# Optimization experiments

Hardware: AMD Instinct MI355X
Metric: run time of the kernel (lower is better)

Reference implementation:

```python
import jax, jax.numpy as jnp
import numpy as np

BETA = 0.25
ALPHA = 0.5
K = 1024
D = 64


def setup_inputs() -> dict:
    key = jax.random.key(0)
    k1, k2 = jax.random.split(key)
    latents = jax.random.normal(k1, (32, D, 64, 64), dtype=jnp.float32)  # NCHW
    # nn.Embedding init uniform_(-1/K, 1/K)
    emb_weight = jax.random.uniform(k2, (K, D), dtype=jnp.float32, minval=-1.0 / K, maxval=1.0 / K)
    return {"latents": latents, "emb_weight": emb_weight}


def reference(latents, emb_weight):
    # NCHW -> NHWC
    x = jnp.transpose(latents, (0, 2, 3, 1))  # [B,H,W,D]
    B, H, W, Dd = x.shape
    flat = x.reshape(-1, Dd)  # [N,D]

    dist = (jnp.sum(flat * flat, axis=1, keepdims=True)
            + jnp.sum(emb_weight * emb_weight, axis=1)
            - 2.0 * flat @ emb_weight.T)
    inds = jnp.argmin(dist, axis=1)  # [N]

    # one-hot @ W == gather
    q = emb_weight[inds].reshape(B, H, W, Dd)

    commitment_loss = jnp.mean((jax.lax.stop_gradient(q) - x) ** 2)
    embedding_loss = jnp.mean((q - jax.lax.stop_gradient(x)) ** 2)
    vq_loss = commitment_loss * BETA + embedding_loss * ALPHA

    alpha_q = 2.0 * ALPHA / (B * H * W * Dd)
    q_st = x + alpha_q * q + jax.lax.stop_gradient((1.0 - alpha_q) * q - x)

    out = jnp.transpose(q_st, (0, 3, 1, 2))  # NHWC -> NCHW
    return out, vq_loss, inds.reshape(B, H, W)
```

## Files before the change

kernel.cpp:

```cpp
#include <hip/hip_runtime.h>

typedef __attribute__((ext_vector_type(8))) short bf16x8;
typedef __attribute__((ext_vector_type(4))) float f32x4;
typedef __attribute__((ext_vector_type(4))) int   i32x4;

#define NROWS     131072
#define KCODES    1024
#define OUT_ELEMS 8388608
#define RPB       64
#define NBLK      2048
#define MAGICF    12582912.0f
#define MARGIN    240
#define XSTRIDE   67
#define WS_PART   0
#define WS_SE     (16*1024)
#define WS_SEM    (20*1024)
#define WS_BPREP  (24*1024)

__device__ __forceinline__ float pairwise64_sq(const float* __restrict__ v) {
#pragma clang fp contract(off)
    float r[8];
#pragma unroll
    for (int j = 0; j < 8; ++j) r[j] = v[j] * v[j];
#pragma unroll
    for (int i = 8; i < 64; i += 8) {
#pragma unroll
        for (int j = 0; j < 8; ++j) r[j] += v[i + j] * v[i + j];
    }
    return ((r[0] + r[1]) + (r[2] + r[3])) + ((r[4] + r[5]) + (r[6] + r[7]));
}

__device__ __forceinline__ int med3i(int a, int b, int c) {
    int mn = min(a, b), mx = max(a, b);
    return max(mn, min(mx, c));
}

__device__ __forceinline__ unsigned short rne_bf16(float v) {
    unsigned u = __float_as_uint(v);
    return (unsigned short)((u + 0x7fffu + ((u >> 16) & 1u)) >> 16);
}

__global__ __launch_bounds__(256) void vq_prep(
    const float* __restrict__ emb, float* __restrict__ se,
    float* __restrict__ sem, unsigned short* __restrict__ bprep)
{
#pragma clang fp contract(off)
    const int k = blockIdx.x * 256 + threadIdx.x;
    if (k >= KCODES) return;
    const float* e = emb + (k << 6);
    float s = pairwise64_sq(e);
    se[k]  = s;
    sem[k] = (s * 65536.0f) + MAGICF;

    const int c = k >> 4, slot = k & 15;
#pragma unroll
    for (int f = 0; f < 2; ++f) {
#pragma unroll
        for (int g = 0; g < 4; ++g) {
            unsigned short h[8];
#pragma unroll
            for (int j = 0; j < 8; ++j)
                h[j] = rne_bf16(e[f * 32 + g * 8 + j] * 256.0f);
            int4 w;
            w.x = h[0] | (h[1] << 16); w.y = h[2] | (h[3] << 16);
            w.z = h[4] | (h[5] << 16); w.w = h[6] | (h[7] << 16);
            *reinterpret_cast<int4*>(bprep + (((c * 2 + f) * 64 + (g * 16 + slot)) << 3)) = w;
        }
    }
}

__global__ __launch_bounds__(256, 2) void vq_main(
    const float* __restrict__ lat, const float* __restrict__ emb,
    const float* __restrict__ se_g, const float* __restrict__ sem_g,
    const unsigned short* __restrict__ bprep,
    float* __restrict__ out, double* __restrict__ partials)
{
#pragma clang fp contract(off)
    __shared__ float  x_lds[RPB * XSTRIDE];
    __shared__ float  se_lds[KCODES];
    __shared__ float  sem_lds[KCODES];
    __shared__ int    keys_lds[RPB * 49];
    __shared__ int    idx_lds[RPB];
    __shared__ double wsum[4];

    const int tid = threadIdx.x, l = tid & 63, wv = tid >> 6;
    const int blk = blockIdx.x;
    const int n0 = blk * RPB, b = n0 >> 12, hw0 = n0 & 4095;
    const float* latb = lat + ((size_t)b << 18) + hw0;

    {
        const int row = tid & 63, dbase = (tid >> 6) * 16;
#pragma unroll
        for (int dd = 0; dd < 16; ++dd) {
            int d = dbase + dd;
            x_lds[row * XSTRIDE + d] = latb[((size_t)d << 12) + row];
        }
    }
    for (int i = tid; i < KCODES; i += 256) { se_lds[i] = se_g[i]; sem_lds[i] = sem_g[i]; }
    __syncthreads();

    bf16x8 afrag[2];
    {
        const int arow = l & 15, kb = (l >> 4) << 3;
        const float* xr = x_lds + (wv * 16 + arow) * XSTRIDE;
#pragma unroll
        for (int kh = 0; kh < 2; ++kh) {
            bf16x8 f;
#pragma unroll
            for (int j = 0; j < 8; ++j)
                f[j] = (short)rne_bf16(xr[kh * 32 + kb + j] * -512.0f);
            afrag[kh] = f;
        }
    }

    int m1[4], m2[4], m3[4];
#pragma unroll
    for (int r = 0; r < 4; ++r) { m1[r] = m2[r] = m3[r] = 0x7fffffff; }

    const i32x4* bp = reinterpret_cast<const i32x4*>(bprep);
    i32x4 bbuf[2][2];
    bbuf[0][0] = bp[l];
    bbuf[0][1] = bp[64 + l];

#pragma unroll 2
    for (int c = 0; c < 64; ++c) {
        const int cur = c & 1, nxt = cur ^ 1;
        if (c < 63) {
            bbuf[nxt][0] = bp[(c + 1) * 128 + l];
            bbuf[nxt][1] = bp[(c + 1) * 128 + 64 + l];
        }
        const float sevm = sem_lds[c * 16 + (l & 15)];
        bf16x8 b0 = __builtin_bit_cast(bf16x8, bbuf[cur][0]);
        bf16x8 b1 = __builtin_bit_cast(bf16x8, bbuf[cur][1]);
        const unsigned code0 = (unsigned)((c << 4) + (l & 15));
        f32x4 acc = {0.f, 0.f, 0.f, 0.f};
        acc = __builtin_amdgcn_mfma_f32_16x16x32_bf16(afrag[0], b0, acc, 0, 0, 0);
        acc = __builtin_amdgcn_mfma_f32_16x16x32_bf16(afrag[1], b1, acc, 0, 0, 0);
#pragma unroll
        for (int r = 0; r < 4; ++r) {
            float uf = acc[r] + sevm;
            int key = (int)((__float_as_uint(uf) << 10) | code0);
            int n1 = min(key, m1[r]);
            int n2 = med3i(key, m1[r], m2[r]);
            int n3 = med3i(max(key, m1[r]), m2[r], m3[r]);
            m1[r] = n1; m2[r] = n2; m3[r] = n3;
        }
    }

#pragma unroll
    for (int r = 0; r < 4; ++r) {
        const int rloc = wv * 16 + ((l >> 4) << 2) + r;
        keys_lds[rloc * 49 + (l & 15) * 3 + 0] = m1[r];
        keys_lds[rloc * 49 + (l & 15) * 3 + 1] = m2[r];
        keys_lds[rloc * 49 + (l & 15) * 3 + 2] = m3[r];
    }
    __syncthreads();

    {
        const int row = tid >> 2, h = tid & 3;
        const int kbase = row * 49 + h * 12;
        int mk = 0x7fffffff;
#pragma unroll
        for (int i = 0; i < 12; ++i) mk = min(mk, keys_lds[kbase + i]);
        mk = min(mk, __shfl_xor(mk, 1, 64));
        mk = min(mk, __shfl_xor(mk, 2, 64));
        const int lim = mk + (MARGIN << 10) + 1023;

        const float* xr = x_lds + row * XSTRIDE;
        float rr0 = 0.0f, rr1 = 0.0f;
#pragma unroll
        for (int i = 0; i < 64; i += 8) {
            float v0 = xr[i + 2 * h];
            float v1 = xr[i + 2 * h + 1];
            rr0 += v0 * v0;
            rr1 += v1 * v1;
        }
        float s_h = rr0 + rr1;
        float p   = s_h + __shfl_xor(s_h, 1, 64);
        float sx  = p + __shfl_xor(p, 2, 64);

        float bestd = 3.4e38f; int besti = KCODES;
#pragma unroll 4
        for (int i = 0; i < 12; ++i) {
            int key = keys_lds[kbase + i];
            if (key <= lim) {
                int code = key & 1023;
                const float* e = emb + (code << 6);
                float g = 0.0f;
#pragma unroll
                for (int d = 0; d < 64; ++d)
                    g = fmaf(xr[d], e[d], g);
                float ss   = sx + se_lds[code];
                float dist = ss - 2.0f * g;
                if (dist < bestd || (dist == bestd && code < besti)) { bestd = dist; besti = code; }
            }
        }
#pragma unroll
        for (int off = 1; off <= 2; off <<= 1) {
            float od = __shfl_xor(bestd, off, 64);
            int   oi = __shfl_xor(besti, off, 64);
            if (od < bestd || (od == bestd && oi < besti)) { bestd = od; besti = oi; }
        }
        if (h == 0) {
            idx_lds[row] = besti;
            out[OUT_ELEMS + 1 + (size_t)n0 + row] = (float)besti;
        }
    }
    __syncthreads();

    double lsum = 0.0;
    {
        const float aq = 1.0f / 8388608.0f;
        const int row = tid & 63, dh = (tid >> 6) * 16;
        const int code = idx_lds[row];
        const float4* eq4 = reinterpret_cast<const float4*>(emb + (code << 6) + dh);
        const float* xr = x_lds + row * XSTRIDE;
        float* ob = out + ((size_t)b << 18) + hw0 + row;
#pragma unroll
        for (int qq = 0; qq < 4; ++qq) {
            float4 qv = eq4[qq];
            float qa[4] = {qv.x, qv.y, qv.z, qv.w};
#pragma unroll
            for (int u = 0; u < 4; ++u) {
                int d = dh + qq * 4 + u;
                float xv = xr[d];
                float qd = qa[u];
                float v  = (xv + aq * qd) + ((1.0f - aq) * qd - xv);
                ob[(size_t)d << 12] = v;
                float diff = qd - xv;
                lsum += (double)diff * (double)diff;
            }
        }
    }

#pragma unroll
    for (int off = 32; off > 0; off >>= 1) lsum += __shfl_down(lsum, off, 64);
    if (l == 0) wsum[wv] = lsum;
    __syncthreads();
    if (tid == 0) partials[blk] = (wsum[0] + wsum[1]) + (wsum[2] + wsum[3]);
}

__global__ __launch_bounds__(512) void vq_finish(
    const double* __restrict__ partials, float* __restrict__ out)
{
    __shared__ double lds[8];
    const int t = threadIdx.x;
    double s = ((partials[t] + partials[t + 512]) + partials[t + 1024]) + partials[t + 1536];
#pragma unroll
    for (int off = 32; off > 0; off >>= 1) s += __shfl_down(s, off, 64);
    if ((t & 63) == 0) lds[t >> 6] = s;
    __syncthreads();
    if (t == 0) {
        double tot = 0.0;
#pragma unroll
        for (int i = 0; i < 8; ++i) tot += lds[i];
        out[OUT_ELEMS] = (float)(0.75 * tot / (double)OUT_ELEMS);
    }
}

extern "C" void kernel_launch(void* const* d_in, const int* in_sizes, int n_in,
                              void* d_out, int out_size, void* d_ws, size_t ws_size,
                              hipStream_t stream)
{
    const float* lat = (const float*)d_in[0];
    const float* emb = (const float*)d_in[1];
    float* out = (float*)d_out;
    char* ws = (char*)d_ws;

    double* partials      = (double*)(ws + WS_PART);
    float* se             = (float*)(ws + WS_SE);
    float* sem            = (float*)(ws + WS_SEM);
    unsigned short* bprep = (unsigned short*)(ws + WS_BPREP);

    vq_prep<<<dim3(4),    dim3(256), 0, stream>>>(emb, se, sem, bprep);
    vq_main<<<dim3(NBLK), dim3(256), 0, stream>>>(lat, emb, se, sem, bprep, out, partials);
    vq_finish<<<dim3(1),  dim3(512), 0, stream>>>(partials, out);
}
```

Baseline: 97.02 us.

## Stage codebook tiles into LDS with async global_load_lds double buffering

```diff
diff --git a/kernel.cpp b/kernel.cpp
--- a/kernel.cpp
+++ b/kernel.cpp
@@ -14,7 +14,7 @@
 #define XSTRIDE   67
 #define WS_PART   0
 #define WS_SE     (16*1024)
-#define WS_SEM    (20*1024)
+#define WS_SEMG   (20*1024)
 #define WS_BPREP  (24*1024)
 
 __device__ __forceinline__ float pairwise64_sq(const float* __restrict__ v) {
@@ -42,15 +42,15 @@
 
 __global__ __launch_bounds__(256) void vq_prep(
     const float* __restrict__ emb, float* __restrict__ se,
-    float* __restrict__ sem, unsigned short* __restrict__ bprep)
+    float* __restrict__ semg, unsigned short* __restrict__ bprep)
 {
 #pragma clang fp contract(off)
     const int k = blockIdx.x * 256 + threadIdx.x;
     if (k >= KCODES) return;
     const float* e = emb + (k << 6);
     float s = pairwise64_sq(e);
-    se[k]  = s;
-    sem[k] = (s * 65536.0f) + MAGICF;
+    se[k]   = s;
+    semg[k] = MAGICF + s * 65536.0f;
 
     const int c = k >> 4, slot = k & 15;
 #pragma unroll
@@ -71,15 +71,14 @@
 
 __global__ __launch_bounds__(256, 2) void vq_main(
     const float* __restrict__ lat, const float* __restrict__ emb,
-    const float* __restrict__ se_g, const float* __restrict__ sem_g,
+    const float* __restrict__ se_g, const float* __restrict__ semg_g,
     const unsigned short* __restrict__ bprep,
     float* __restrict__ out, double* __restrict__ partials)
 {
 #pragma clang fp contract(off)
     __shared__ float  x_lds[RPB * XSTRIDE];
-    __shared__ float  se_lds[KCODES];
-    __shared__ float  sem_lds[KCODES];
     __shared__ int    keys_lds[RPB * 49];
+    __shared__ i32x4  stage4[512];
     __shared__ int    idx_lds[RPB];
     __shared__ double wsum[4];
 
@@ -87,6 +86,15 @@
     const int blk = blockIdx.x;
     const int n0 = blk * RPB, b = n0 >> 12, hw0 = n0 & 4095;
     const float* latb = lat + ((size_t)b << 18) + hw0;
+    const char* bpb = (const char*)bprep;
+    const int scol = l & 15;
+
+#define STAGE(P, S)                                                              \
+    __builtin_amdgcn_global_load_lds(                                            \
+        (const __attribute__((address_space(1))) unsigned int*)                  \
+            (bpb + ((P) * 4096 + wv * 1024 + l * 16)),                           \
+        (__attribute__((address_space(3))) unsigned int*)                        \
+            (&stage4[(S) * 256 + wv * 64]), 16, 0, 0)
 
     {
         const int row = tid & 63, dbase = (tid >> 6) * 16;
@@ -96,56 +104,70 @@
             x_lds[row * XSTRIDE + d] = latb[((size_t)d << 12) + row];
         }
     }
-    for (int i = tid; i < KCODES; i += 256) { se_lds[i] = se_g[i]; sem_lds[i] = sem_g[i]; }
-    __syncthreads();
-
-    bf16x8 afrag[2];
+    STAGE(0, 0);
+    __syncthreads();
+
+    bf16x8 afrag0, afrag1;
     {
         const int arow = l & 15, kb = (l >> 4) << 3;
         const float* xr = x_lds + (wv * 16 + arow) * XSTRIDE;
-#pragma unroll
-        for (int kh = 0; kh < 2; ++kh) {
-            bf16x8 f;
-#pragma unroll
-            for (int j = 0; j < 8; ++j)
-                f[j] = (short)rne_bf16(xr[kh * 32 + kb + j] * -512.0f);
-            afrag[kh] = f;
-        }
+        bf16x8 f;
+#pragma unroll
+        for (int j = 0; j < 8; ++j) f[j] = (short)rne_bf16(xr[kb + j]      * -512.0f);
+        afrag0 = f;
+#pragma unroll
+        for (int j = 0; j < 8; ++j) f[j] = (short)rne_bf16(xr[32 + kb + j] * -512.0f);
+        afrag1 = f;
     }
 
     int m1[4], m2[4], m3[4];
 #pragma unroll
     for (int r = 0; r < 4; ++r) { m1[r] = m2[r] = m3[r] = 0x7fffffff; }
 
-    const i32x4* bp = reinterpret_cast<const i32x4*>(bprep);
-    i32x4 bbuf[2][2];
-    bbuf[0][0] = bp[l];
-    bbuf[0][1] = bp[64 + l];
-
-#pragma unroll 2
-    for (int c = 0; c < 64; ++c) {
-        const int cur = c & 1, nxt = cur ^ 1;
-        if (c < 63) {
-            bbuf[nxt][0] = bp[(c + 1) * 128 + l];
-            bbuf[nxt][1] = bp[(c + 1) * 128 + 64 + l];
-        }
-        const float sevm = sem_lds[c * 16 + (l & 15)];
-        bf16x8 b0 = __builtin_bit_cast(bf16x8, bbuf[cur][0]);
-        bf16x8 b1 = __builtin_bit_cast(bf16x8, bbuf[cur][1]);
-        const unsigned code0 = (unsigned)((c << 4) + (l & 15));
-        f32x4 acc = {0.f, 0.f, 0.f, 0.f};
-        acc = __builtin_amdgcn_mfma_f32_16x16x32_bf16(afrag[0], b0, acc, 0, 0, 0);
-        acc = __builtin_amdgcn_mfma_f32_16x16x32_bf16(afrag[1], b1, acc, 0, 0, 0);
-#pragma unroll
-        for (int r = 0; r < 4; ++r) {
-            float uf = acc[r] + sevm;
-            int key = (int)((__float_as_uint(uf) << 10) | code0);
-            int n1 = min(key, m1[r]);
-            int n2 = med3i(key, m1[r], m2[r]);
-            int n3 = med3i(max(key, m1[r]), m2[r], m3[r]);
-            m1[r] = n1; m2[r] = n2; m3[r] = n3;
-        }
-    }
+    float svA0 = semg_g[scol],            svB0 = semg_g[16 + scol];
+    float svA1 = semg_g[32 + scol],       svB1 = semg_g[48 + scol];
+
+#define CHUNK(S, CI, CC, SV)                                                          \
+    {   i32x4 B0 = stage4[(S) * 256 + (CI) * 128 + l];                                \
+        i32x4 B1 = stage4[(S) * 256 + (CI) * 128 + 64 + l];                           \
+        bf16x8 b0_ = __builtin_bit_cast(bf16x8, B0);                                  \
+        bf16x8 b1_ = __builtin_bit_cast(bf16x8, B1);                                  \
+        const unsigned code0_ = (unsigned)(((CC) << 4) + scol);                       \
+        f32x4 acc = {SV, SV, SV, SV};                                                 \
+        acc = __builtin_amdgcn_mfma_f32_16x16x32_bf16(afrag0, b0_, acc, 0, 0, 0);     \
+        acc = __builtin_amdgcn_mfma_f32_16x16x32_bf16(afrag1, b1_, acc, 0, 0, 0);     \
+        _Pragma("unroll")                                                             \
+        for (int r = 0; r < 4; ++r) {                                                 \
+            int key = (int)((__float_as_uint(acc[r]) << 10) | code0_);                \
+            int n1 = min(key, m1[r]);                                                 \
+            int n2 = med3i(key, m1[r], m2[r]);                                        \
+            int n3 = med3i(max(key, m1[r]), m2[r], m3[r]);                            \
+            m1[r] = n1; m2[r] = n2; m3[r] = n3;                                       \
+        }                                                                             \
+    }
+
+#pragma unroll 1
+    for (int p = 0; p < 32; p += 2) {
+        if (p + 1 < 32) STAGE(p + 1, 1);
+        CHUNK(0, 0, 2 * p,     svA0);
+        CHUNK(0, 1, 2 * p + 1, svB0);
+        if (p + 2 < 32) {
+            svA0 = semg_g[(2 * p + 4) * 16 + scol];
+            svB0 = semg_g[(2 * p + 5) * 16 + scol];
+        }
+        __syncthreads();
+
+        if (p + 2 < 32) STAGE(p + 2, 0);
+        CHUNK(1, 0, 2 * p + 2, svA1);
+        CHUNK(1, 1, 2 * p + 3, svB1);
+        if (p + 3 < 32) {
+            svA1 = semg_g[(2 * p + 6) * 16 + scol];
+            svB1 = semg_g[(2 * p + 7) * 16 + scol];
+        }
+        __syncthreads();
+    }
+#undef CHUNK
+#undef STAGE
 
 #pragma unroll
     for (int r = 0; r < 4; ++r) {
@@ -176,8 +198,8 @@
             rr1 += v1 * v1;
         }
         float s_h = rr0 + rr1;
-        float p   = s_h + __shfl_xor(s_h, 1, 64);
-        float sx  = p + __shfl_xor(p, 2, 64);
+        float pq  = s_h + __shfl_xor(s_h, 1, 64);
+        float sx  = pq + __shfl_xor(pq, 2, 64);
 
         float bestd = 3.4e38f; int besti = KCODES;
 #pragma unroll 4
@@ -190,7 +212,7 @@
 #pragma unroll
                 for (int d = 0; d < 64; ++d)
                     g = fmaf(xr[d], e[d], g);
-                float ss   = sx + se_lds[code];
+                float ss   = sx + se_g[code];
                 float dist = ss - 2.0f * g;
                 if (dist < bestd || (dist == bestd && code < besti)) { bestd = dist; besti = code; }
             }
@@ -269,10 +291,10 @@
 
     double* partials      = (double*)(ws + WS_PART);
     float* se             = (float*)(ws + WS_SE);
-    float* sem            = (float*)(ws + WS_SEM);
+    float* semg           = (float*)(ws + WS_SEMG);
     unsigned short* bprep = (unsigned short*)(ws + WS_BPREP);
 
-    vq_prep<<<dim3(4),    dim3(256), 0, stream>>>(emb, se, sem, bprep);
-    vq_main<<<dim3(NBLK), dim3(256), 0, stream>>>(lat, emb, se, sem, bprep, out, partials);
+    vq_prep<<<dim3(4),    dim3(256), 0, stream>>>(emb, se, semg, bprep);
+    vq_main<<<dim3(NBLK), dim3(256), 0, stream>>>(lat, emb, se, semg, bprep, out, partials);
     vq_finish<<<dim3(1),  dim3(512), 0, stream>>>(partials, out);
 }
```

Result: faster. 92.02 us (-5.2%).
